# Optimization experiments

Measured on AMD Instinct MI355X. Metric: run time of the kernel, lower is better.

## Reference

```python
import jax, jax.numpy as jnp
import numpy as np

N = 50000      # nodes
E = 800000     # edges (before self-loops)
DIN = 384
D = 128        # hidden_dim == output_dim
H = 4          # heads
FH = D // H    # per-head dim
B = 64         # graphs in batch
NEG = 0.2      # LeakyReLU slope in GATConv
EPS = 1e-5     # LayerNorm eps


def setup_inputs() -> dict:
    key = jax.random.key(0)
    ks = jax.random.split(key, 24)
    s = 0.02
    inp = {
        'node_features': jax.random.normal(ks[0], (N, DIN), jnp.float32),
        'edge_index': jax.random.randint(ks[1], (2, E), 0, N, dtype=jnp.int64),
        'edge_weight': jax.random.uniform(ks[2], (E,), jnp.float32),
        'batch': jnp.sort(jax.random.randint(ks[3], (N,), 0, B, dtype=jnp.int64)),
        # input projection
        'Wp': jax.random.normal(ks[4], (DIN, D), jnp.float32) * s,
        'bp': jnp.zeros((D,), jnp.float32),
    }
    for l in range(2):
        o = 5 + l * 9
        inp[f'W{l}'] = jax.random.normal(ks[o], (D, D), jnp.float32) * s      # lin_src (shared src/dst)
        inp[f'as{l}'] = jax.random.normal(ks[o + 1], (H, FH), jnp.float32) * s  # att_src
        inp[f'ad{l}'] = jax.random.normal(ks[o + 2], (H, FH), jnp.float32) * s  # att_dst
        inp[f'We{l}'] = jax.random.normal(ks[o + 3], (D,), jnp.float32) * s   # lin_edge (edge_dim=1)
        inp[f'ae{l}'] = jax.random.normal(ks[o + 4], (H, FH), jnp.float32) * s  # att_edge
        inp[f'b{l}'] = jnp.zeros((D,), jnp.float32)                           # GATConv bias
        inp[f'g{l}'] = jnp.ones((D,), jnp.float32)                            # LayerNorm gamma
        inp[f'be{l}'] = jnp.zeros((D,), jnp.float32)                          # LayerNorm beta
    return inp


def _gat(x, src, dst, ew, W, a_s, a_d, We, a_e, b):
    """PyG GATConv(in, D/H, heads=H, edge_dim=1), eval mode. ew includes self-loops."""
    n = x.shape[0]
    h = (x @ W).reshape(n, H, FH)                      # [N,H,FH]
    a_src = jnp.einsum('nhf,hf->nh', h, a_s)           # [N,H]
    a_dst = jnp.einsum('nhf,hf->nh', h, a_d)
    e = (ew[:, None] * We[None, :]).reshape(-1, H, FH)  # edge_dim=1 linear, no bias
    a_eg = jnp.einsum('ehf,hf->eh', e, a_e)            # [E,H]
    alpha = jax.nn.leaky_relu(a_src[src] + a_dst[dst] + a_eg, NEG)
    # softmax over incoming edges of each dst node
    amax = jax.ops.segment_max(alpha, dst, num_segments=n)
    amax = jnp.where(jnp.isfinite(amax), amax, 0.0)
    ex = jnp.exp(alpha - amax[dst])
    denom = jax.ops.segment_sum(ex, dst, num_segments=n)
    coef = ex / (denom[dst] + 1e-16)                   # [E,H]
    msg = h[src] * coef[..., None]                     # [E,H,FH]
    out = jax.ops.segment_sum(msg, dst, num_segments=n).reshape(n, D)
    return out + b


def _ln(x, g, b):
    mu = x.mean(-1, keepdims=True)
    v = ((x - mu) ** 2).mean(-1, keepdims=True)
    return (x - mu) * jax.lax.rsqrt(v + EPS) * g + b


def reference(node_features, edge_index, edge_weight, batch, Wp, bp,
              W0, as0, ad0, We0, ae0, b0, g0, be0,
              W1, as1, ad1, We1, ae1, b1, g1, be1):
    n = node_features.shape[0]
    # PyG GATConv add_self_loops=True, fill_value='mean' for edge_attr
    loop = jnp.arange(n, dtype=edge_index.dtype)
    src = jnp.concatenate([edge_index[0], loop])
    dst = jnp.concatenate([edge_index[1], loop])
    ew = jnp.concatenate([edge_weight, jnp.full((n,), edge_weight.mean(), edge_weight.dtype)])

    x = node_features @ Wp + bp
    for (W, a_s, a_d, We, a_e, b, g, be) in (
        (W0, as0, ad0, We0, ae0, b0, g0, be0),
        (W1, as1, ad1, We1, ae1, b1, g1, be1),
    ):
        res = x
        y = _gat(x, src, dst, ew, W, a_s, a_d, We, a_e, b)
        y = jax.nn.elu(_ln(y, g, be))
        x = y + res  # shapes match (hidden == output)

    # global_mean_pool
    s = jax.ops.segment_sum(x, batch, num_segments=B)
    c = jax.ops.segment_sum(jnp.ones((n,), x.dtype), batch, num_segments=B)
    return s / jnp.maximum(c, 1.0)[:, None]
```

## Files before the change

### kernel.cpp

```cpp
#include <hip/hip_runtime.h>

#define N_NODES 50000
#define N_EDGES 800000
#define DIN 384
#define DH 128
#define NB 64
#define NEG 0.2f

__device__ __forceinline__ float bf2f(unsigned short u) {
    return __uint_as_float((unsigned)u << 16);
}
__device__ __forceinline__ unsigned short f2bf(float x) {
    unsigned u = __float_as_uint(x);
    return (unsigned short)((u + 0x7fff + ((u >> 16) & 1)) >> 16);
}
__device__ __forceinline__ float sel4(float4 v, int k) {
    float r = v.x;
    r = (k == 1) ? v.y : r;
    r = (k == 2) ? v.z : r;
    r = (k == 3) ? v.w : r;
    return r;
}
using us8 = __attribute__((ext_vector_type(8))) unsigned short;
using short8 = __attribute__((ext_vector_type(8))) short;
using f32x4  = __attribute__((ext_vector_type(4))) float;

__global__ __launch_bounds__(256) void histew_kernel(const int* __restrict__ dst,
                                                     const float* __restrict__ ew,
                                                     int* __restrict__ cnt,
                                                     int* __restrict__ rank,
                                                     float* __restrict__ ews,
                                                     const float* __restrict__ Wp,
                                                     const float* __restrict__ W0,
                                                     const float* __restrict__ W1,
                                                     unsigned short* __restrict__ Wtp,
                                                     unsigned short* __restrict__ Wt0,
                                                     unsigned short* __restrict__ Wt1) {
    __shared__ float sred[4];
    const int tid = threadIdx.x;
    const int pi = blockIdx.x * 256 + tid;
    if (blockIdx.x < 192) {
        const int k = pi >> 7, n = pi & 127;
        Wtp[(size_t)n * DIN + k] = f2bf(Wp[pi]);
        if (pi < DH * DH) {
            Wt0[(size_t)n * DH + k] = f2bf(W0[pi]);
            Wt1[(size_t)n * DH + k] = f2bf(W1[pi]);
        }
    }
    float v = 0.0f;
    for (int i = blockIdx.x * 256 + tid; i < N_EDGES; i += gridDim.x * 256) {
        rank[i] = atomicAdd(&cnt[dst[i]], 1);
        v += ew[i];
    }
    #pragma unroll
    for (int o = 32; o; o >>= 1) v += __shfl_down(v, o, 64);
    if ((tid & 63) == 0) sred[tid >> 6] = v;
    __syncthreads();
    if (tid == 0) atomicAdd(ews, sred[0] + sred[1] + sred[2] + sred[3]);
}

#define SB 196
__global__ __launch_bounds__(256) void scan_a(const int* __restrict__ cnt,
                       int* __restrict__ scanned, int* __restrict__ bsums,
                       const float* __restrict__ We0, const float* __restrict__ ae0,
                       const float* __restrict__ We1, const float* __restrict__ ae1,
                       const float* __restrict__ ews, float* __restrict__ consts) {
    __shared__ int s[256];
    const int tid = threadIdx.x;
    if (blockIdx.x < SB) {
        int i = blockIdx.x * 256 + tid;
        int v = (i < N_NODES) ? cnt[i] : 0;
        s[tid] = v; __syncthreads();
        for (int o = 1; o < 256; o <<= 1) {
            int t = (tid >= o) ? s[tid - o] : 0;
            __syncthreads();
            s[tid] += t;
            __syncthreads();
        }
        if (i < N_NODES) scanned[i] = s[tid] - v;
        if (tid == 255) bsums[blockIdx.x] = s[255];
    } else if (tid < 64) {
        const int l = tid;
        float p00 = We0[l] * ae0[l];
        float p01 = We0[l + 64] * ae0[l + 64];
        float p10 = We1[l] * ae1[l];
        float p11 = We1[l + 64] * ae1[l + 64];
        #pragma unroll
        for (int o = 1; o < 32; o <<= 1) {
            p00 += __shfl_xor(p00, o, 64); p01 += __shfl_xor(p01, o, 64);
            p10 += __shfl_xor(p10, o, 64); p11 += __shfl_xor(p11, o, 64);
        }
        const float c0 = __shfl(p00, 0, 64), c1 = __shfl(p00, 32, 64);
        const float c2 = __shfl(p01, 0, 64), c3 = __shfl(p01, 32, 64);
        const float d0 = __shfl(p10, 0, 64), d1 = __shfl(p10, 32, 64);
        const float d2 = __shfl(p11, 0, 64), d3 = __shfl(p11, 32, 64);
        if (l == 0) {
            consts[0] = c0; consts[1] = c1; consts[2] = c2; consts[3] = c3;
            consts[4] = d0; consts[5] = d1; consts[6] = d2; consts[7] = d3;
            consts[8] = ews[0] * (1.0f / N_EDGES);
        }
    }
}

__global__ __launch_bounds__(256) void scan_bc(const int* __restrict__ scanned,
                        const int* __restrict__ bsums,
                        const int* __restrict__ cnt, int* __restrict__ ptr) {
    __shared__ int red[4];
    const int tid = threadIdx.x;
    int part = 0;
    for (int j = tid; j < blockIdx.x; j += 256) part += bsums[j];
    #pragma unroll
    for (int o = 32; o; o >>= 1) part += __shfl_down(part, o, 64);
    if ((tid & 63) == 0) red[tid >> 6] = part;
    __syncthreads();
    const int off = red[0] + red[1] + red[2] + red[3];
    const int i = blockIdx.x * 256 + tid;
    if (i < N_NODES) {
        const int p = scanned[i] + off;
        ptr[i] = p;
        if (i == N_NODES - 1) ptr[N_NODES] = p + cnt[i];
    }
}

#define PROJB 391
__global__ __launch_bounds__(256) void fillproj_kernel(
    const int* __restrict__ src, const int* __restrict__ dst,
    const float* __restrict__ ew, const int* __restrict__ rank,
    const int* __restrict__ ptr, int2* __restrict__ recE,
    const float* __restrict__ A, const unsigned short* __restrict__ Wt,
    const float* __restrict__ bias, float* __restrict__ C,
    unsigned short* __restrict__ Cb, int M)
{
    constexpr int K = DIN, BM = 128, BK = 32, LS = 40;
    __shared__ unsigned short As[BM * LS];
    __shared__ unsigned short Bs[DH * LS];
    const int tid = threadIdx.x;

    if (blockIdx.x >= PROJB) {
        const int e0 = ((blockIdx.x - PROJB) * 256 + tid) * 4;
        if (e0 >= N_EDGES) return;
        const int4 d4 = *(const int4*)(dst + e0);
        const int4 s4 = *(const int4*)(src + e0);
        const int4 r4 = *(const int4*)(rank + e0);
        const float4 w4 = *(const float4*)(ew + e0);
        recE[ptr[d4.x] + r4.x] = make_int2(s4.x, __float_as_int(w4.x));
        recE[ptr[d4.y] + r4.y] = make_int2(s4.y, __float_as_int(w4.y));
        recE[ptr[d4.z] + r4.z] = make_int2(s4.z, __float_as_int(w4.z));
        recE[ptr[d4.w] + r4.w] = make_int2(s4.w, __float_as_int(w4.w));
        return;
    }

    const int w = tid >> 6, l = tid & 63;
    const int lane16 = l & 15, quad = l >> 4;
    const int m0 = blockIdx.x * BM;

    f32x4 acc[2][8] = {};

    const int ar = tid >> 1, ah = tid & 1;
    int arow = m0 + ar; if (arow >= M) arow = M - 1;
    const float* Ap = A + (size_t)arow * K;

    for (int k0 = 0; k0 < K; k0 += BK) {
        __syncthreads();
        #pragma unroll
        for (int j = 0; j < 4; ++j) {
            float4 v = *(const float4*)(Ap + k0 + ah * 16 + j * 4);
            ushort4 u = {f2bf(v.x), f2bf(v.y), f2bf(v.z), f2bf(v.w)};
            *(ushort4*)&As[ar * LS + ah * 16 + j * 4] = u;
        }
        #pragma unroll
        for (int i = 0; i < 2; ++i) {
            const int idx = tid + 256 * i;
            const int bn = idx >> 2, seg = idx & 3;
            us8 v = *(const us8*)(Wt + (size_t)bn * K + k0 + seg * 8);
            *(us8*)&Bs[bn * LS + seg * 8] = v;
        }
        __syncthreads();
        short8 af0 = *(short8*)&As[(w * 32 + lane16) * LS + quad * 8];
        short8 af1 = *(short8*)&As[(w * 32 + 16 + lane16) * LS + quad * 8];
        #pragma unroll
        for (int nt = 0; nt < 8; ++nt) {
            short8 bf = *(short8*)&Bs[(nt * 16 + lane16) * LS + quad * 8];
            acc[0][nt] = __builtin_amdgcn_mfma_f32_16x16x32_bf16(af0, bf, acc[0][nt], 0, 0, 0);
            acc[1][nt] = __builtin_amdgcn_mfma_f32_16x16x32_bf16(af1, bf, acc[1][nt], 0, 0, 0);
        }
    }

    #pragma unroll
    for (int r2 = 0; r2 < 2; ++r2) {
        const int orow0 = m0 + w * 32 + r2 * 16 + quad * 4;
        #pragma unroll
        for (int nt = 0; nt < 8; ++nt) {
            const int col = nt * 16 + lane16;
            const float bv = bias[col];
            #pragma unroll
            for (int r = 0; r < 4; ++r) {
                const int row = orow0 + r;
                if (row < M) {
                    const float v = acc[r2][nt][r] + bv;
                    C[(size_t)row * DH + col] = v;
                    Cb[(size_t)row * DH + col] = f2bf(v);
                }
            }
        }
    }
}

__global__ __launch_bounds__(256) void mfma_gemm_layer(
    const unsigned short* __restrict__ Ab, const unsigned short* __restrict__ Wt,
    unsigned short* __restrict__ Hout, int M,
    const float* __restrict__ a_s, const float* __restrict__ a_d,
    float* __restrict__ asrc_o, float* __restrict__ adst_o)
{
    constexpr int K = DH, BM = 64, BK = 32, LS = 40;
    __shared__ unsigned short As[BM * LS];
    __shared__ unsigned short Bs[DH * LS];

    const int tid = threadIdx.x;
    const int w = tid >> 6, l = tid & 63;
    const int lane16 = l & 15, quad = l >> 4;
    const int m0 = blockIdx.x * BM;

    f32x4 acc[8] = {};

    const int ar = tid >> 2, aseg = tid & 3;
    int arow = m0 + ar; if (arow >= M) arow = M - 1;
    const unsigned short* Ap = Ab + (size_t)arow * K;

    for (int k0 = 0; k0 < K; k0 += BK) {
        __syncthreads();
        {
            us8 v = *(const us8*)(Ap + k0 + aseg * 8);
            *(us8*)&As[ar * LS + aseg * 8] = v;
        }
        #pragma unroll
        for (int i = 0; i < 2; ++i) {
            const int idx = tid + 256 * i;
            const int bn = idx >> 2, seg = idx & 3;
            us8 v = *(const us8*)(Wt + (size_t)bn * K + k0 + seg * 8);
            *(us8*)&Bs[bn * LS + seg * 8] = v;
        }
        __syncthreads();
        short8 af = *(short8*)&As[(w * 16 + lane16) * LS + quad * 8];
        #pragma unroll
        for (int nt = 0; nt < 8; ++nt) {
            short8 bf = *(short8*)&Bs[(nt * 16 + lane16) * LS + quad * 8];
            acc[nt] = __builtin_amdgcn_mfma_f32_16x16x32_bf16(af, bf, acc[nt], 0, 0, 0);
        }
    }

    const int orow0 = m0 + w * 16 + quad * 4;
    #pragma unroll
    for (int nt = 0; nt < 8; ++nt) {
        const int col = nt * 16 + lane16;
        #pragma unroll
        for (int r = 0; r < 4; ++r) {
            const int row = orow0 + r;
            if (row < M)
                Hout[(size_t)row * DH + col] = f2bf(acc[nt][r]);
        }
    }

    float psh[4][4] = {}, pdh[4][4] = {};
    #pragma unroll
    for (int nt = 0; nt < 8; ++nt) {
        const int hd = nt >> 1;
        const float asv = a_s[nt * 16 + lane16];
        const float adv = a_d[nt * 16 + lane16];
        #pragma unroll
        for (int r = 0; r < 4; ++r) {
            psh[hd][r] = fmaf(acc[nt][r], asv, psh[hd][r]);
            pdh[hd][r] = fmaf(acc[nt][r], adv, pdh[hd][r]);
        }
    }
    #pragma unroll
    for (int o = 1; o < 16; o <<= 1) {
        #pragma unroll
        for (int hd = 0; hd < 4; ++hd)
            #pragma unroll
            for (int r = 0; r < 4; ++r) {
                psh[hd][r] += __shfl_xor(psh[hd][r], o, 64);
                pdh[hd][r] += __shfl_xor(pdh[hd][r], o, 64);
            }
    }
    if (lane16 == 0) {
        #pragma unroll
        for (int r = 0; r < 4; ++r) {
            const int row = orow0 + r;
            if (row < M) {
                float4 o1 = {psh[0][r], psh[1][r], psh[2][r], psh[3][r]};
                float4 o2 = {pdh[0][r], pdh[1][r], pdh[2][r], pdh[3][r]};
                *(float4*)(asrc_o + (size_t)row * 4) = o1;
                *(float4*)(adst_o + (size_t)row * 4) = o2;
            }
        }
    }
}

#define MSG_NPB 16
template<bool POOL>
__global__ __launch_bounds__(256) void msg_kernel(
    const unsigned short* __restrict__ h, const float* __restrict__ asrc,
    const float* __restrict__ adst, const float* __restrict__ xres,
    const int* __restrict__ indptr, const int2* __restrict__ recE,
    const float* __restrict__ consts, const int layer,
    const float* __restrict__ bias, const float* __restrict__ gamma,
    const float* __restrict__ beta, float* __restrict__ xout,
    unsigned short* __restrict__ xob,
    const int* __restrict__ batch, float* __restrict__ pool,
    int* __restrict__ gcnt)
{
    __shared__ float pacc[16][DH];
    __shared__ int sb[16], firstb[16], scnt[16], nsl;

    const int l = threadIdx.x & 63;
    const int wv = threadIdx.x >> 6;
    const int grp = l >> 4;
    const int c8 = l & 15;
    const int hd8 = c8 >> 2;

    const int ninb = wv * 4 + grp;
    const int n = blockIdx.x * MSG_NPB + ninb;

    if constexpr (POOL) {
        if (c8 == 0) sb[ninb] = batch[n];
        for (int t = threadIdx.x; t < 16 * DH; t += 256) ((float*)pacc)[t] = 0.f;
    }

    const float4 ccv = *(const float4*)(consts + layer * 4);
    const float cc_l = sel4(ccv, hd8);
    const float ewm = consts[8];
    const unsigned short* hb = h + c8 * 8;

    const int st = indptr[n];
    const int deg = indptr[n + 1] - st;
    const float ad_l = adst[(size_t)n * 4 + hd8];
    const float as_l = asrc[(size_t)n * 4 + hd8];

    float a0 = as_l + ad_l + ewm * cc_l;
    a0 = a0 > 0.f ? a0 : NEG * a0;
    const float pv0_l = __expf(a0);

    float dsum = 0.f;
    float acc8[8];
    {
        us8 u = *(const us8*)(hb + (size_t)n * DH);
        #pragma unroll
        for (int i = 0; i < 8; ++i) acc8[i] = pv0_l * bf2f(u[i]);
    }

    const int2* rq = recE + st;
    int e = 0;
    for (; e + 3 < deg; e += 4) {
        const int2 r0 = rq[e],     r1 = rq[e + 1];
        const int2 r2 = rq[e + 2], r3 = rq[e + 3];
        const float av0 = asrc[(size_t)r0.x * 4 + hd8];
        const float av1 = asrc[(size_t)r1.x * 4 + hd8];
        const float av2 = asrc[(size_t)r2.x * 4 + hd8];
        const float av3 = asrc[(size_t)r3.x * 4 + hd8];
        us8 u0 = *(const us8*)(hb + (size_t)r0.x * DH);
        us8 u1 = *(const us8*)(hb + (size_t)r1.x * DH);
        us8 u2 = *(const us8*)(hb + (size_t)r2.x * DH);
        us8 u3 = *(const us8*)(hb + (size_t)r3.x * DH);
        float al0 = av0 + ad_l + __int_as_float(r0.y) * cc_l;
        float al1 = av1 + ad_l + __int_as_float(r1.y) * cc_l;
        float al2 = av2 + ad_l + __int_as_float(r2.y) * cc_l;
        float al3 = av3 + ad_l + __int_as_float(r3.y) * cc_l;
        al0 = al0 > 0.f ? al0 : NEG * al0;
        al1 = al1 > 0.f ? al1 : NEG * al1;
        al2 = al2 > 0.f ? al2 : NEG * al2;
        al3 = al3 > 0.f ? al3 : NEG * al3;
        const float c0 = __expf(al0), c1 = __expf(al1);
        const float c2 = __expf(al2), c3 = __expf(al3);
        dsum += (c0 + c1) + (c2 + c3);
        #pragma unroll
        for (int i = 0; i < 8; ++i)
            acc8[i] = fmaf(c0, bf2f(u0[i]),
                      fmaf(c1, bf2f(u1[i]),
                      fmaf(c2, bf2f(u2[i]),
                      fmaf(c3, bf2f(u3[i]), acc8[i]))));
    }
    for (; e < deg; ++e) {
        const int2 r = rq[e];
        const float av = asrc[(size_t)r.x * 4 + hd8];
        us8 u = *(const us8*)(hb + (size_t)r.x * DH);
        float al = av + ad_l + __int_as_float(r.y) * cc_l;
        al = al > 0.f ? al : NEG * al;
        const float c = __expf(al);
        dsum += c;
        #pragma unroll
        for (int i = 0; i < 8; ++i) acc8[i] = fmaf(c, bf2f(u[i]), acc8[i]);
    }

    const float inv_d = 1.0f / (dsum + pv0_l + 1e-16f);
    const float4 b4a = *(const float4*)(bias + c8 * 8);
    const float4 b4b = *(const float4*)(bias + c8 * 8 + 4);
    float y[8];
    y[0] = acc8[0] * inv_d + b4a.x; y[1] = acc8[1] * inv_d + b4a.y;
    y[2] = acc8[2] * inv_d + b4a.z; y[3] = acc8[3] * inv_d + b4a.w;
    y[4] = acc8[4] * inv_d + b4b.x; y[5] = acc8[5] * inv_d + b4b.y;
    y[6] = acc8[6] * inv_d + b4b.z; y[7] = acc8[7] * inv_d + b4b.w;

    float s1 = 0.f, s2 = 0.f;
    #pragma unroll
    for (int i = 0; i < 8; ++i) { s1 += y[i]; s2 += y[i] * y[i]; }
    #pragma unroll
    for (int o = 1; o < 16; o <<= 1) {
        s1 += __shfl_xor(s1, o, 64);
        s2 += __shfl_xor(s2, o, 64);
    }
    const float mu = s1 * (1.0f / DH);
    const float var = s2 * (1.0f / DH) - mu * mu;
    const float rs = rsqrtf(var + 1e-5f);

    const float4 g4a = *(const float4*)(gamma + c8 * 8);
    const float4 g4b = *(const float4*)(gamma + c8 * 8 + 4);
    const float4 e4a = *(const float4*)(beta + c8 * 8);
    const float4 e4b = *(const float4*)(beta + c8 * 8 + 4);
    const float4 r4a = *(const float4*)(xres + (size_t)n * DH + c8 * 8);
    const float4 r4b = *(const float4*)(xres + (size_t)n * DH + c8 * 8 + 4);
    const float gv[8] = {g4a.x, g4a.y, g4a.z, g4a.w, g4b.x, g4b.y, g4b.z, g4b.w};
    const float ev[8] = {e4a.x, e4a.y, e4a.z, e4a.w, e4b.x, e4b.y, e4b.z, e4b.w};
    const float rv[8] = {r4a.x, r4a.y, r4a.z, r4a.w, r4b.x, r4b.y, r4b.z, r4b.w};
    float z[8];
    #pragma unroll
    for (int i = 0; i < 8; ++i) {
        float t = (y[i] - mu) * rs * gv[i] + ev[i];
        z[i] = (t > 0.f ? t : __expf(t) - 1.0f) + rv[i];
    }

    if constexpr (!POOL) {
        *(float4*)(xout + (size_t)n * DH + c8 * 8)     = *(float4*)&z[0];
        *(float4*)(xout + (size_t)n * DH + c8 * 8 + 4) = *(float4*)&z[4];
        ushort4 ub0 = {f2bf(z[0]), f2bf(z[1]), f2bf(z[2]), f2bf(z[3])};
        ushort4 ub1 = {f2bf(z[4]), f2bf(z[5]), f2bf(z[6]), f2bf(z[7])};
        *(ushort4*)(xob + (size_t)n * DH + c8 * 8)     = ub0;
        *(ushort4*)(xob + (size_t)n * DH + c8 * 8 + 4) = ub1;
    } else {
        __syncthreads();
        int slot = 0;
        #pragma unroll 1
        for (int j = 1; j <= ninb; ++j) slot += (sb[j] != sb[j - 1]);
        #pragma unroll
        for (int k = 0; k < 8; ++k) atomicAdd(&pacc[slot][c8 * 8 + k], z[k]);
        if (threadIdx.x == 0) {
            int s = 0, c = 1;
            firstb[0] = sb[0];
            for (int j = 1; j < 16; ++j) {
                if (sb[j] != sb[j - 1]) { scnt[s] = c; ++s; firstb[s] = sb[j]; c = 1; }
                else ++c;
            }
            scnt[s] = c; nsl = s + 1;
        }
        __syncthreads();
        const int ns = nsl;
        for (int s = 0; s < ns; ++s) {
            if (threadIdx.x < DH)
                atomicAdd(&pool[(size_t)firstb[s] * DH + threadIdx.x], pacc[s][threadIdx.x]);
            if (threadIdx.x == 0)
                atomicAdd(&gcnt[firstb[s]], scnt[s]);
        }
    }
}

__global__ void div_kernel(const float* __restrict__ pool, const int* __restrict__ gcnt,
                           float* __restrict__ out)
{
    int i = blockIdx.x * blockDim.x + threadIdx.x;
    if (i < NB * DH) {
        float c = (float)gcnt[i >> 7];
        out[i] = pool[i] / fmaxf(c, 1.0f);
    }
}

extern "C" void kernel_launch(void* const* d_in, const int* in_sizes, int n_in,
                              void* d_out, int out_size, void* d_ws, size_t ws_size,
                              hipStream_t stream)
{
    const float* nf    = (const float*)d_in[0];
    const int*   esrc  = (const int*)d_in[1];
    const int*   edst  = esrc + N_EDGES;
    const float* ew    = (const float*)d_in[2];
    const int*   batch = (const int*)d_in[3];
    const float* Wp    = (const float*)d_in[4];
    const float* bp    = (const float*)d_in[5];
    const float* Wl[2]  = {(const float*)d_in[6],  (const float*)d_in[14]};
    const float* asl[2] = {(const float*)d_in[7],  (const float*)d_in[15]};
    const float* adl[2] = {(const float*)d_in[8],  (const float*)d_in[16]};
    const float* Wel[2] = {(const float*)d_in[9],  (const float*)d_in[17]};
    const float* ael[2] = {(const float*)d_in[10], (const float*)d_in[18]};
    const float* bl[2]  = {(const float*)d_in[11], (const float*)d_in[19]};
    const float* gl[2]  = {(const float*)d_in[12], (const float*)d_in[20]};
    const float* bel[2] = {(const float*)d_in[13], (const float*)d_in[21]};
    float* outp = (float*)d_out;

    char* w = (char*)d_ws;
    auto alloc = [&](size_t bytes) { char* p = w; w += (bytes + 255) & ~255ull; return p; };
    float* xA     = (float*)alloc((size_t)N_NODES * DH * 4);
    float* xB     = (float*)alloc((size_t)N_NODES * DH * 4);
    unsigned short* hbuf = (unsigned short*)alloc((size_t)N_NODES * DH * 2);
    unsigned short* xb   = (unsigned short*)alloc((size_t)N_NODES * DH * 2);
    float* asrc   = (float*)alloc((size_t)N_NODES * 4 * 4);
    float* adst   = (float*)alloc((size_t)N_NODES * 4 * 4);
    float* pool   = (float*)alloc((size_t)NB * DH * 4);
    int* gcnt     = (int*)alloc(256);
    float* ews    = (float*)alloc(256);
    int* cnt      = (int*)alloc((size_t)N_NODES * 4);
    int* scanned  = (int*)alloc((size_t)N_NODES * 4);
    int* bsums    = (int*)alloc(1024);
    int* ptr      = (int*)alloc((size_t)(N_NODES + 8) * 4);
    int* rank     = (int*)alloc((size_t)N_EDGES * 4);
    int2* recE    = (int2*)alloc((size_t)N_EDGES * 8);
    float* consts = (float*)alloc(256);
    unsigned short* Wtp = (unsigned short*)alloc((size_t)DH * DIN * 2);
    unsigned short* Wt0 = (unsigned short*)alloc((size_t)DH * DH * 2);
    unsigned short* Wt1 = (unsigned short*)alloc((size_t)DH * DH * 2);
    unsigned short* Wts[2] = {Wt0, Wt1};

    hipMemsetAsync(pool, 0, (size_t)NB * DH * 4 + 256 + 256 + (size_t)N_NODES * 4, stream);

    histew_kernel<<<1024, 256, 0, stream>>>(edst, ew, cnt, rank, ews,
                                            Wp, Wl[0], Wl[1], Wtp, Wt0, Wt1);
    scan_a<<<SB + 1, 256, 0, stream>>>(cnt, scanned, bsums,
                                       Wel[0], ael[0], Wel[1], ael[1], ews, consts);
    scan_bc<<<SB, 256, 0, stream>>>(scanned, bsums, cnt, ptr);
    fillproj_kernel<<<PROJB + (N_EDGES / 4 + 255) / 256, 256, 0, stream>>>(
        esrc, edst, ew, rank, ptr, recE, nf, Wtp, bp, xA, xb, N_NODES);

    const int gb = (N_NODES + 63) / 64;
    const int mb = N_NODES / MSG_NPB;

    mfma_gemm_layer<<<gb, 256, 0, stream>>>(xb, Wts[0], hbuf, N_NODES,
                                            asl[0], adl[0], asrc, adst);
    msg_kernel<false><<<mb, 256, 0, stream>>>(
        hbuf, asrc, adst, xA, ptr, recE, consts, 0,
        bl[0], gl[0], bel[0], xB, xb, nullptr, nullptr, nullptr);

    mfma_gemm_layer<<<gb, 256, 0, stream>>>(xb, Wts[1], hbuf, N_NODES,
                                            asl[1], adl[1], asrc, adst);
    msg_kernel<true><<<mb, 256, 0, stream>>>(
        hbuf, asrc, adst, xB, ptr, recE, consts, 1,
        bl[1], gl[1], bel[1], nullptr, nullptr, batch, pool, gcnt);

    div_kernel<<<(NB * DH + 255) / 256, 256, 0, stream>>>(pool, gcnt, outp);
}
```

Baseline: 379.6 us.

## Fold attention vectors into GEMM weights and restructure pooling into per-wave accumulation

Precomputes W·a_src and W·a_dst per head as 8 extra bf16 weight columns, so the GEMM produces the attention logits through a ninth MFMA tile. This replaces the post-GEMM FMA and shuffle reduction epilogue. The final message kernel now handles 16 nodes per wave in a loop and accumulates same-graph sums in registers before issuing atomics, replacing the shared-memory slot scheme with its block syncs. Computing the logits from bf16-rounded folded weights changes their precision slightly, and the pool kernel launches a quarter as many blocks, which lowers parallelism.

Result: faster. 359.0 us (-5.4%).

```diff
diff --git a/kernel.cpp b/kernel.cpp
--- a/kernel.cpp
+++ b/kernel.cpp
@@ -26,16 +26,14 @@
 using f32x4  = __attribute__((ext_vector_type(4))) float;
 
 __global__ __launch_bounds__(256) void histew_kernel(const int* __restrict__ dst,
-                                                     const float* __restrict__ ew,
-                                                     int* __restrict__ cnt,
-                                                     int* __restrict__ rank,
-                                                     float* __restrict__ ews,
-                                                     const float* __restrict__ Wp,
-                                                     const float* __restrict__ W0,
-                                                     const float* __restrict__ W1,
-                                                     unsigned short* __restrict__ Wtp,
-                                                     unsigned short* __restrict__ Wt0,
-                                                     unsigned short* __restrict__ Wt1) {
+        const float* __restrict__ ew, int* __restrict__ cnt,
+        int* __restrict__ rank, float* __restrict__ ews,
+        const float* __restrict__ Wp, const float* __restrict__ W0,
+        const float* __restrict__ W1,
+        const float* __restrict__ as0, const float* __restrict__ ad0,
+        const float* __restrict__ as1, const float* __restrict__ ad1,
+        unsigned short* __restrict__ Wtp, unsigned short* __restrict__ Wt0,
+        unsigned short* __restrict__ Wt1) {
     __shared__ float sred[4];
     const int tid = threadIdx.x;
     const int pi = blockIdx.x * 256 + tid;
@@ -45,6 +43,21 @@
         if (pi < DH * DH) {
             Wt0[(size_t)n * DH + k] = f2bf(W0[pi]);
             Wt1[(size_t)n * DH + k] = f2bf(W1[pi]);
+        }
+    } else if (blockIdx.x < 196) {
+        const int b = blockIdx.x - 192;
+        const int layer = b >> 1, sd = b & 1;
+        const float* Ws = layer ? W1 : W0;
+        const float* av = layer ? (sd ? ad1 : as1) : (sd ? ad0 : as0);
+        unsigned short* Wt = layer ? Wt1 : Wt0;
+        #pragma unroll
+        for (int rep = 0; rep < 2; ++rep) {
+            const int idx = rep * 256 + tid;
+            const int k = idx >> 2, hd = idx & 3;
+            float s = 0.f;
+            for (int f = 0; f < 32; ++f)
+                s += Ws[k * DH + hd * 32 + f] * av[hd * 32 + f];
+            Wt[(size_t)(128 + sd * 4 + hd) * DH + k] = f2bf(s);
         }
     }
     float v = 0.0f;
@@ -209,19 +222,18 @@
 __global__ __launch_bounds__(256) void mfma_gemm_layer(
     const unsigned short* __restrict__ Ab, const unsigned short* __restrict__ Wt,
     unsigned short* __restrict__ Hout, int M,
-    const float* __restrict__ a_s, const float* __restrict__ a_d,
     float* __restrict__ asrc_o, float* __restrict__ adst_o)
 {
     constexpr int K = DH, BM = 64, BK = 32, LS = 40;
     __shared__ unsigned short As[BM * LS];
-    __shared__ unsigned short Bs[DH * LS];
+    __shared__ unsigned short Bs[144 * LS];
 
     const int tid = threadIdx.x;
     const int w = tid >> 6, l = tid & 63;
     const int lane16 = l & 15, quad = l >> 4;
     const int m0 = blockIdx.x * BM;
 
-    f32x4 acc[8] = {};
+    f32x4 acc[9] = {};
 
     const int ar = tid >> 2, aseg = tid & 3;
     int arow = m0 + ar; if (arow >= M) arow = M - 1;
@@ -234,16 +246,18 @@
             *(us8*)&As[ar * LS + aseg * 8] = v;
         }
         #pragma unroll
-        for (int i = 0; i < 2; ++i) {
+        for (int i = 0; i < 3; ++i) {
             const int idx = tid + 256 * i;
-            const int bn = idx >> 2, seg = idx & 3;
-            us8 v = *(const us8*)(Wt + (size_t)bn * K + k0 + seg * 8);
-            *(us8*)&Bs[bn * LS + seg * 8] = v;
+            if (idx < 576) {
+                const int bn = idx >> 2, seg = idx & 3;
+                us8 v = *(const us8*)(Wt + (size_t)bn * K + k0 + seg * 8);
+                *(us8*)&Bs[bn * LS + seg * 8] = v;
+            }
         }
         __syncthreads();
         short8 af = *(short8*)&As[(w * 16 + lane16) * LS + quad * 8];
         #pragma unroll
-        for (int nt = 0; nt < 8; ++nt) {
+        for (int nt = 0; nt < 9; ++nt) {
             short8 bf = *(short8*)&Bs[(nt * 16 + lane16) * LS + quad * 8];
             acc[nt] = __builtin_amdgcn_mfma_f32_16x16x32_bf16(af, bf, acc[nt], 0, 0, 0);
         }
@@ -260,78 +274,27 @@
                 Hout[(size_t)row * DH + col] = f2bf(acc[nt][r]);
         }
     }
-
-    float psh[4][4] = {}, pdh[4][4] = {};
-    #pragma unroll
-    for (int nt = 0; nt < 8; ++nt) {
-        const int hd = nt >> 1;
-        const float asv = a_s[nt * 16 + lane16];
-        const float adv = a_d[nt * 16 + lane16];
-        #pragma unroll
-        for (int r = 0; r < 4; ++r) {
-            psh[hd][r] = fmaf(acc[nt][r], asv, psh[hd][r]);
-            pdh[hd][r] = fmaf(acc[nt][r], adv, pdh[hd][r]);
-        }
-    }
-    #pragma unroll
-    for (int o = 1; o < 16; o <<= 1) {
-        #pragma unroll
-        for (int hd = 0; hd < 4; ++hd)
-            #pragma unroll
-            for (int r = 0; r < 4; ++r) {
-                psh[hd][r] += __shfl_xor(psh[hd][r], o, 64);
-                pdh[hd][r] += __shfl_xor(pdh[hd][r], o, 64);
-            }
-    }
-    if (lane16 == 0) {
-        #pragma unroll
-        for (int r = 0; r < 4; ++r) {
-            const int row = orow0 + r;
-            if (row < M) {
-                float4 o1 = {psh[0][r], psh[1][r], psh[2][r], psh[3][r]};
-                float4 o2 = {pdh[0][r], pdh[1][r], pdh[2][r], pdh[3][r]};
-                *(float4*)(asrc_o + (size_t)row * 4) = o1;
-                *(float4*)(adst_o + (size_t)row * 4) = o2;
-            }
-        }
-    }
-}
-
-#define MSG_NPB 16
-template<bool POOL>
-__global__ __launch_bounds__(256) void msg_kernel(
-    const unsigned short* __restrict__ h, const float* __restrict__ asrc,
-    const float* __restrict__ adst, const float* __restrict__ xres,
+    #pragma unroll
+    for (int r = 0; r < 4; ++r) {
+        const int row = orow0 + r;
+        if (row < M && lane16 < 8) {
+            if (lane16 < 4) asrc_o[(size_t)row * 4 + lane16] = acc[8][r];
+            else            adst_o[(size_t)row * 4 + (lane16 - 4)] = acc[8][r];
+        }
+    }
+}
+
+__device__ __forceinline__ void msg_node(
+    const int n, const int c8, const int hd8,
+    const float cc_l, const float ewm,
+    const unsigned short* __restrict__ h,
+    const float* __restrict__ asrc, const float* __restrict__ adst,
+    const float* __restrict__ xres,
     const int* __restrict__ indptr, const int2* __restrict__ recE,
-    const float* __restrict__ consts, const int layer,
     const float* __restrict__ bias, const float* __restrict__ gamma,
-    const float* __restrict__ beta, float* __restrict__ xout,
-    unsigned short* __restrict__ xob,
-    const int* __restrict__ batch, float* __restrict__ pool,
-    int* __restrict__ gcnt)
-{
-    __shared__ float pacc[16][DH];
-    __shared__ int sb[16], firstb[16], scnt[16], nsl;
-
-    const int l = threadIdx.x & 63;
-    const int wv = threadIdx.x >> 6;
-    const int grp = l >> 4;
-    const int c8 = l & 15;
-    const int hd8 = c8 >> 2;
-
-    const int ninb = wv * 4 + grp;
-    const int n = blockIdx.x * MSG_NPB + ninb;
-
-    if constexpr (POOL) {
-        if (c8 == 0) sb[ninb] = batch[n];
-        for (int t = threadIdx.x; t < 16 * DH; t += 256) ((float*)pacc)[t] = 0.f;
-    }
-
-    const float4 ccv = *(const float4*)(consts + layer * 4);
-    const float cc_l = sel4(ccv, hd8);
-    const float ewm = consts[8];
+    const float* __restrict__ beta, float z[8])
+{
     const unsigned short* hb = h + c8 * 8;
-
     const int st = indptr[n];
     const int deg = indptr[n + 1] - st;
     const float ad_l = adst[(size_t)n * 4 + hd8];
@@ -422,44 +385,111 @@
     const float gv[8] = {g4a.x, g4a.y, g4a.z, g4a.w, g4b.x, g4b.y, g4b.z, g4b.w};
     const float ev[8] = {e4a.x, e4a.y, e4a.z, e4a.w, e4b.x, e4b.y, e4b.z, e4b.w};
     const float rv[8] = {r4a.x, r4a.y, r4a.z, r4a.w, r4b.x, r4b.y, r4b.z, r4b.w};
-    float z[8];
     #pragma unroll
     for (int i = 0; i < 8; ++i) {
         float t = (y[i] - mu) * rs * gv[i] + ev[i];
         z[i] = (t > 0.f ? t : __expf(t) - 1.0f) + rv[i];
     }
-
-    if constexpr (!POOL) {
-        *(float4*)(xout + (size_t)n * DH + c8 * 8)     = *(float4*)&z[0];
-        *(float4*)(xout + (size_t)n * DH + c8 * 8 + 4) = *(float4*)&z[4];
-        ushort4 ub0 = {f2bf(z[0]), f2bf(z[1]), f2bf(z[2]), f2bf(z[3])};
-        ushort4 ub1 = {f2bf(z[4]), f2bf(z[5]), f2bf(z[6]), f2bf(z[7])};
-        *(ushort4*)(xob + (size_t)n * DH + c8 * 8)     = ub0;
-        *(ushort4*)(xob + (size_t)n * DH + c8 * 8 + 4) = ub1;
-    } else {
-        __syncthreads();
-        int slot = 0;
-        #pragma unroll 1
-        for (int j = 1; j <= ninb; ++j) slot += (sb[j] != sb[j - 1]);
-        #pragma unroll
-        for (int k = 0; k < 8; ++k) atomicAdd(&pacc[slot][c8 * 8 + k], z[k]);
-        if (threadIdx.x == 0) {
-            int s = 0, c = 1;
-            firstb[0] = sb[0];
-            for (int j = 1; j < 16; ++j) {
-                if (sb[j] != sb[j - 1]) { scnt[s] = c; ++s; firstb[s] = sb[j]; c = 1; }
-                else ++c;
+}
+
+#define MSG_NPB 16
+__global__ __launch_bounds__(256) void msg_main_kernel(
+    const unsigned short* __restrict__ h, const float* __restrict__ asrc,
+    const float* __restrict__ adst, const float* __restrict__ xres,
+    const int* __restrict__ indptr, const int2* __restrict__ recE,
+    const float* __restrict__ consts,
+    const float* __restrict__ bias, const float* __restrict__ gamma,
+    const float* __restrict__ beta, float* __restrict__ xout,
+    unsigned short* __restrict__ xob)
+{
+    const int l = threadIdx.x & 63;
+    const int wv = threadIdx.x >> 6;
+    const int grp = l >> 4, c8 = l & 15, hd8 = c8 >> 2;
+    const int n = blockIdx.x * MSG_NPB + wv * 4 + grp;
+
+    const float cc_l = sel4(*(const float4*)(consts + 0), hd8);
+    const float ewm = consts[8];
+
+    float z[8];
+    msg_node(n, c8, hd8, cc_l, ewm, h, asrc, adst, xres, indptr, recE,
+             bias, gamma, beta, z);
+
+    *(float4*)(xout + (size_t)n * DH + c8 * 8)     = *(float4*)&z[0];
+    *(float4*)(xout + (size_t)n * DH + c8 * 8 + 4) = *(float4*)&z[4];
+    ushort4 ub0 = {f2bf(z[0]), f2bf(z[1]), f2bf(z[2]), f2bf(z[3])};
+    ushort4 ub1 = {f2bf(z[4]), f2bf(z[5]), f2bf(z[6]), f2bf(z[7])};
+    *(ushort4*)(xob + (size_t)n * DH + c8 * 8)     = ub0;
+    *(ushort4*)(xob + (size_t)n * DH + c8 * 8 + 4) = ub1;
+}
+
+__global__ __launch_bounds__(256) void msg_pool_kernel(
+    const unsigned short* __restrict__ h, const float* __restrict__ asrc,
+    const float* __restrict__ adst, const float* __restrict__ xres,
+    const int* __restrict__ indptr, const int2* __restrict__ recE,
+    const float* __restrict__ consts,
+    const float* __restrict__ bias, const float* __restrict__ gamma,
+    const float* __restrict__ beta, const int* __restrict__ batch,
+    float* __restrict__ pool, int* __restrict__ gcnt)
+{
+    const int l = threadIdx.x & 63;
+    const int wv = threadIdx.x >> 6;
+    const int grp = l >> 4, c8 = l & 15, hd8 = c8 >> 2;
+    const int base = (blockIdx.x * 4 + wv) * 16;
+    if (base >= N_NODES) return;
+
+    const float cc_l = sel4(*(const float4*)(consts + 4), hd8);
+    const float ewm = consts[8];
+
+    float zacc[8] = {};
+    int curb = batch[base];
+    int ncnt = 0;
+
+    for (int t = 0; t < 4; ++t) {
+        const int n = base + t * 4 + grp;
+        float z[8];
+        msg_node(n, c8, hd8, cc_l, ewm, h, asrc, adst, xres, indptr, recE,
+                 bias, gamma, beta, z);
+        const int bmy = batch[n];
+        if (__all(bmy == curb)) {
+            #pragma unroll
+            for (int i = 0; i < 8; ++i) zacc[i] += z[i];
+            ncnt += 4;
+        } else {
+            if (ncnt > 0) {
+                #pragma unroll
+                for (int i = 0; i < 8; ++i) {
+                    zacc[i] += __shfl_xor(zacc[i], 16, 64);
+                    zacc[i] += __shfl_xor(zacc[i], 32, 64);
+                }
+                if (grp == 0) {
+                    #pragma unroll
+                    for (int i = 0; i < 8; ++i)
+                        atomicAdd(&pool[(size_t)curb * DH + c8 * 8 + i], zacc[i]);
+                }
+                if (l == 0) atomicAdd(&gcnt[curb], ncnt);
             }
-            scnt[s] = c; nsl = s + 1;
-        }
-        __syncthreads();
-        const int ns = nsl;
-        for (int s = 0; s < ns; ++s) {
-            if (threadIdx.x < DH)
-                atomicAdd(&pool[(size_t)firstb[s] * DH + threadIdx.x], pacc[s][threadIdx.x]);
-            if (threadIdx.x == 0)
-                atomicAdd(&gcnt[firstb[s]], scnt[s]);
-        }
+            #pragma unroll
+            for (int i = 0; i < 8; ++i) zacc[i] = 0.f;
+            ncnt = 0;
+            #pragma unroll
+            for (int i = 0; i < 8; ++i)
+                atomicAdd(&pool[(size_t)bmy * DH + c8 * 8 + i], z[i]);
+            if (c8 == 0) atomicAdd(&gcnt[bmy], 1);
+            curb = __shfl(bmy, 48, 64);
+        }
+    }
+    if (ncnt > 0) {
+        #pragma unroll
+        for (int i = 0; i < 8; ++i) {
+            zacc[i] += __shfl_xor(zacc[i], 16, 64);
+            zacc[i] += __shfl_xor(zacc[i], 32, 64);
+        }
+        if (grp == 0) {
+            #pragma unroll
+            for (int i = 0; i < 8; ++i)
+                atomicAdd(&pool[(size_t)curb * DH + c8 * 8 + i], zacc[i]);
+        }
+        if (l == 0) atomicAdd(&gcnt[curb], ncnt);
     }
 }
 
@@ -513,14 +543,16 @@
     int2* recE    = (int2*)alloc((size_t)N_EDGES * 8);
     float* consts = (float*)alloc(256);
     unsigned short* Wtp = (unsigned short*)alloc((size_t)DH * DIN * 2);
-    unsigned short* Wt0 = (unsigned short*)alloc((size_t)DH * DH * 2);
-    unsigned short* Wt1 = (unsigned short*)alloc((size_t)DH * DH * 2);
+    unsigned short* Wt0 = (unsigned short*)alloc((size_t)144 * DH * 2);
+    unsigned short* Wt1 = (unsigned short*)alloc((size_t)144 * DH * 2);
     unsigned short* Wts[2] = {Wt0, Wt1};
 
     hipMemsetAsync(pool, 0, (size_t)NB * DH * 4 + 256 + 256 + (size_t)N_NODES * 4, stream);
 
     histew_kernel<<<1024, 256, 0, stream>>>(edst, ew, cnt, rank, ews,
-                                            Wp, Wl[0], Wl[1], Wtp, Wt0, Wt1);
+                                            Wp, Wl[0], Wl[1],
+                                            asl[0], adl[0], asl[1], adl[1],
+                                            Wtp, Wt0, Wt1);
     scan_a<<<SB + 1, 256, 0, stream>>>(cnt, scanned, bsums,
                                        Wel[0], ael[0], Wel[1], ael[1], ews, consts);
     scan_bc<<<SB, 256, 0, stream>>>(scanned, bsums, cnt, ptr);
@@ -530,17 +562,15 @@
     const int gb = (N_NODES + 63) / 64;
     const int mb = N_NODES / MSG_NPB;
 
-    mfma_gemm_layer<<<gb, 256, 0, stream>>>(xb, Wts[0], hbuf, N_NODES,
-                                            asl[0], adl[0], asrc, adst);
-    msg_kernel<false><<<mb, 256, 0, stream>>>(
-        hbuf, asrc, adst, xA, ptr, recE, consts, 0,
-        bl[0], gl[0], bel[0], xB, xb, nullptr, nullptr, nullptr);
-
-    mfma_gemm_layer<<<gb, 256, 0, stream>>>(xb, Wts[1], hbuf, N_NODES,
-                                            asl[1], adl[1], asrc, adst);
-    msg_kernel<true><<<mb, 256, 0, stream>>>(
-        hbuf, asrc, adst, xB, ptr, recE, consts, 1,
-        bl[1], gl[1], bel[1], nullptr, nullptr, batch, pool, gcnt);
+    mfma_gemm_layer<<<gb, 256, 0, stream>>>(xb, Wts[0], hbuf, N_NODES, asrc, adst);
+    msg_main_kernel<<<mb, 256, 0, stream>>>(
+        hbuf, asrc, adst, xA, ptr, recE, consts,
+        bl[0], gl[0], bel[0], xB, xb);
+
+    mfma_gemm_layer<<<gb, 256, 0, stream>>>(xb, Wts[1], hbuf, N_NODES, asrc, adst);
+    msg_pool_kernel<<<(N_NODES / 16 + 3) / 4, 256, 0, stream>>>(
+        hbuf, asrc, adst, xB, ptr, recE, consts,
+        bl[1], gl[1], bel[1], batch, pool, gcnt);
 
     div_kernel<<<(NB * DH + 255) / 256, 256, 0, stream>>>(pool, gcnt, outp);
 }
```
